# Kernel tuning notes

Measured on AMD Instinct MI355X. Metric: run time of the kernel, lower is better.

The kernel has to match this reference:

```python
import jax, jax.numpy as jnp
import numpy as np

N, C, CI, H, W = 4, 512, 256, 64, 64  # batch, in_channels, inter_channels, spatial
EPS = 1e-5


def conv1x1(x, w, b):
    # x: (N,C,H,W), w: (O,C), b: (O,)
    return jnp.einsum('nchw,oc->nohw', x, w) + b[None, :, None, None]


def setup_inputs() -> dict:
    key = jax.random.key(0)
    ks = jax.random.split(key, 11)
    s = 0.02
    return {
        'x': jax.random.normal(ks[0], (N, C, H, W), dtype=jnp.float32),
        'g_w': jax.random.normal(ks[1], (CI, C), dtype=jnp.float32) * s,
        'g_b': jax.random.normal(ks[2], (CI,), dtype=jnp.float32) * s,
        'theta_w': jax.random.normal(ks[3], (CI, C), dtype=jnp.float32) * s,
        'theta_b': jax.random.normal(ks[4], (CI,), dtype=jnp.float32) * s,
        'phi_w': jax.random.normal(ks[5], (CI, C), dtype=jnp.float32) * s,
        'phi_b': jax.random.normal(ks[6], (CI,), dtype=jnp.float32) * s,
        'wz_w': jax.random.normal(ks[7], (C, CI), dtype=jnp.float32) * s,
        'wz_b': jax.random.normal(ks[8], (C,), dtype=jnp.float32) * s,
        'bn_gamma': jax.random.normal(ks[9], (C,), dtype=jnp.float32) * 0.1 + 1.0,
        'bn_beta': jax.random.normal(ks[10], (C,), dtype=jnp.float32) * 0.1,
    }


def reference(x, g_w, g_b, theta_w, theta_b, phi_w, phi_b, wz_w, wz_b, bn_gamma, bn_beta):
    # NLBlockND.forward_self, mode='embedded', dimension=2, bn_layer=True
    n = x.shape[0]
    L = x.shape[2] * x.shape[3]  # H*W tokens
    g_x = conv1x1(x, g_w, g_b).reshape(n, CI, L)          # (N,Ci,L)
    theta_x = conv1x1(x, theta_w, theta_b).reshape(n, CI, L)
    phi_x = conv1x1(x, phi_w, phi_b).reshape(n, CI, L)
    f = jnp.einsum('ncl,ncm->nlm', theta_x, phi_x)        # (N,L,L) = theta^T @ phi
    f_div_C = jax.nn.softmax(f, axis=-1)
    y = jnp.einsum('nlm,ncm->ncl', f_div_C, g_x)          # (N,Ci,L) = (attn @ g)^T
    y = y.reshape(n, CI, x.shape[2], x.shape[3])
    w_y = conv1x1(y, wz_w, wz_b)                          # (N,C,H,W)
    # BatchNorm2d, training-mode batch statistics (biased variance)
    mean = jnp.mean(w_y, axis=(0, 2, 3), keepdims=True)
    var = jnp.var(w_y, axis=(0, 2, 3), keepdims=True)
    w_y = (w_y - mean) * jax.lax.rsqrt(var + EPS)
    w_y = w_y * bn_gamma[None, :, None, None] + bn_beta[None, :, None, None]
    return w_y + x
```

## Files before the change

### kernel.cpp

```cpp
#include <hip/hip_runtime.h>
#include <hip/hip_bf16.h>
#include <hip/hip_fp16.h>


#define NB    4
#define CDIM  512
#define CIDIM 256
#define LDIM  4096
#define BN_EPS 1e-5f

typedef unsigned short u16;
typedef __attribute__((ext_vector_type(8))) short short8;
typedef __attribute__((ext_vector_type(4))) float f32x4;
typedef __attribute__((ext_vector_type(16))) float f32x16;

#define WY_OFF    0
#define THPH_OFF  8388608
#define G_OFF     12582912
#define Y_OFF     14680064
#define WTS_OFF   16777216
#define BIAS2_OFF 17039360
#define ML_OFF    17039872
#define ST_OFF    17105408

__device__ __forceinline__ u16 f2b(float f) {
    union { float f; unsigned u; } v; v.f = f;
    return (u16)((v.u + 0x7FFFu + ((v.u >> 16) & 1u)) >> 16);
}

__device__ __forceinline__ float b2f(u16 x) {
    return __uint_as_float((unsigned)x << 16);
}

__device__ __forceinline__ unsigned pack2(float a, float b) {
    return (unsigned)f2b(a) | ((unsigned)f2b(b) << 16);
}

__device__ __forceinline__ void gl_lds16(const u16* g, u16* l) {
    __builtin_amdgcn_global_load_lds(
        (const __attribute__((address_space(1))) void*)g,
        (__attribute__((address_space(3))) void*)l, 16, 0, 0);
}

__global__ void transpose_x(const float* __restrict__ x, u16* __restrict__ xt) {
    __shared__ float tile[32][33];
    int n = blockIdx.z;
    int l0 = blockIdx.x * 32, c0 = blockIdx.y * 32;
    const float* xn = x + (size_t)n * CDIM * LDIM;
    u16* xtn = xt + (size_t)n * LDIM * CDIM;
    int tx = threadIdx.x, ty = threadIdx.y;
#pragma unroll
    for (int k = 0; k < 4; k++)
        tile[ty + 8 * k][tx] = xn[(size_t)(c0 + ty + 8 * k) * LDIM + l0 + tx];
    __syncthreads();
#pragma unroll
    for (int k = 0; k < 4; k++)
        xtn[(size_t)(l0 + ty + 8 * k) * CDIM + c0 + tx] = f2b(tile[tx][ty + 8 * k]);
}

__global__ void cast_w(const float* __restrict__ gw, const float* __restrict__ tw,
                       const float* __restrict__ pw, const float* __restrict__ zw,
                       u16* __restrict__ out) {
    int idx = blockIdx.x * 256 + threadIdx.x;
    if (idx >= 4 * 131072) return;
    int seg = idx >> 17, off = idx & 131071;
    const float* s = (seg == 0) ? gw : (seg == 1) ? tw : (seg == 2) ? pw : zw;
    out[idx] = f2b(s[off]);
}

__global__ void concat_bias(const float* __restrict__ tb, const float* __restrict__ pb,
                            float* __restrict__ out) {
    int i = blockIdx.x * 256 + threadIdx.x;
    if (i < 256) out[i] = tb[i];
    else if (i < 512) out[i] = pb[i - 256];
}

template <int BIAS_MODE, bool OUT_BF16>
__global__ __launch_bounds__(256)
void gemm_nt(const u16* __restrict__ A, const u16* __restrict__ B,
             void* __restrict__ Dv, const float* __restrict__ bias,
             int K, int lda, int ldb, int ldd,
             long batchA, long batchB, long batchD) {
    __shared__ __align__(16) u16 As[128 * 32];
    __shared__ __align__(16) u16 Bs[128 * 32];
    int z = blockIdx.z;
    A += (size_t)z * batchA;
    B += (size_t)z * batchB;

    int tid = threadIdx.x, lane = tid & 63, wave = tid >> 6;
    int n0 = blockIdx.x * 128, m0 = blockIdx.y * 128;
    int wr = wave >> 1, wc = wave & 1;

    f32x4 acc[4][4];
#pragma unroll
    for (int i = 0; i < 4; i++)
#pragma unroll
        for (int j = 0; j < 4; j++) acc[i][j] = (f32x4){0.f, 0.f, 0.f, 0.f};

    int sr = wave * 16 + (lane >> 2);
    int ss = ((lane & 3) ^ ((lane >> 2) & 3)) * 8;
    const u16* Ag0 = A + (size_t)(m0 + sr) * lda + ss;
    const u16* Ag1 = A + (size_t)(m0 + 64 + sr) * lda + ss;
    const u16* Bg0 = B + (size_t)(n0 + sr) * ldb + ss;
    const u16* Bg1 = B + (size_t)(n0 + 64 + sr) * ldb + ss;
    u16* Al0 = &As[(wave * 16) * 32];
    u16* Al1 = &As[(64 + wave * 16) * 32];
    u16* Bl0 = &Bs[(wave * 16) * 32];
    u16* Bl1 = &Bs[(64 + wave * 16) * 32];

    int koff = ((lane >> 4) ^ (lane & 3)) * 8;
    int ra = (wr * 64 + (lane & 15)) * 32 + koff;
    int rb = (wc * 64 + (lane & 15)) * 32 + koff;

    for (int k0 = 0; k0 < K; k0 += 32) {
        __syncthreads();
        gl_lds16(Ag0 + k0, Al0);
        gl_lds16(Ag1 + k0, Al1);
        gl_lds16(Bg0 + k0, Bl0);
        gl_lds16(Bg1 + k0, Bl1);
        __syncthreads();

        short8 af[4], bf[4];
#pragma unroll
        for (int mt = 0; mt < 4; mt++) af[mt] = *(const short8*)&As[ra + mt * 16 * 32];
#pragma unroll
        for (int nt = 0; nt < 4; nt++) bf[nt] = *(const short8*)&Bs[rb + nt * 16 * 32];
#pragma unroll
        for (int mt = 0; mt < 4; mt++)
#pragma unroll
            for (int nt = 0; nt < 4; nt++)
                acc[mt][nt] = __builtin_amdgcn_mfma_f32_16x16x32_bf16(
                    af[mt], bf[nt], acc[mt][nt], 0, 0, 0);
    }

#pragma unroll
    for (int mt = 0; mt < 4; mt++) {
        int mg = m0 + wr * 64 + mt * 16 + (lane >> 4) * 4;
#pragma unroll
        for (int nt = 0; nt < 4; nt++) {
            int ng = n0 + wc * 64 + nt * 16 + (lane & 15);
#pragma unroll
            for (int r = 0; r < 4; r++) {
                float v = acc[mt][nt][r];
                if (BIAS_MODE == 1) v += bias[mg + r];
                if (BIAS_MODE == 2) v += bias[ng];
                if (OUT_BF16) {
                    u16* D = (u16*)Dv + (size_t)z * batchD;
                    D[(size_t)(mg + r) * ldd + ng] = f2b(v);
                } else {
                    float* D = (float*)Dv + (size_t)z * batchD;
                    D[(size_t)(mg + r) * ldd + ng] = v;
                }
            }
        }
    }
}

__global__ __launch_bounds__(256, 2)
void flash_attn(const u16* __restrict__ THPH, const u16* __restrict__ G,
                u16* __restrict__ OPB, unsigned* __restrict__ ML4) {
    __shared__ __align__(16) u16 Ks[64 * 256];
    __shared__ __align__(16) u16 Vs[256 * 64];

    int b = blockIdx.x;
    int n = b & 3;
    int jh = (b >> 2) & 3;
    int qt = b >> 4;
    int q0 = qt * 128;

    const u16* TH = THPH + (size_t)n * LDIM * 512;
    const u16* PH = TH + 256;
    const u16* Gn = G + (size_t)n * LDIM * CIDIM;
    u16* OPh = OPB + ((size_t)jh * NB + n) * CIDIM * LDIM;
    unsigned* MLh = ML4 + ((size_t)jh * NB + n) * LDIM;

    int tid = threadIdx.x, lane = tid & 63, w = tid >> 6;
    int h = lane >> 5, lq = lane & 31, l7 = lane & 7;

    short8 qf[16];
    {
        const u16* qb = TH + (size_t)(q0 + w * 32 + lq) * 512 + h * 8;
#pragma unroll
        for (int c = 0; c < 16; c++) qf[c] = *(const short8*)(qb + c * 16);
    }

    f32x16 o[8];
#pragma unroll
    for (int i = 0; i < 8; i++)
#pragma unroll
        for (int e = 0; e < 16; e++) o[i][e] = 0.f;
    float m = -3e38f, lsum = 0.f;

    int krh = lane >> 5;
    int ksl = lane & 31;
    int vr = lane >> 3;
    int vsl = (lane & 7) ^ vr;

#define STAGE(jt_) do {                                                        \
    int j0_ = (jh * 16 + (jt_)) * 64;                                          \
    _Pragma("unroll")                                                          \
    for (int i = 0; i < 8; i++) {                                              \
        int r = w * 16 + 2 * i + krh;                                          \
        int s = ksl ^ (r & 7);                                                 \
        gl_lds16(PH + (size_t)(j0_ + r) * 512 + s * 8,                         \
                 &Ks[(w * 16 + 2 * i) * 256]);                                 \
    }                                                                          \
    _Pragma("unroll")                                                          \
    for (int i = 0; i < 8; i++) {                                              \
        int r = w * 64 + 8 * i + vr;                                           \
        gl_lds16(Gn + (size_t)r * LDIM + j0_ + vsl * 8,                        \
                 &Vs[(w * 64 + 8 * i) * 64]);                                  \
    }                                                                          \
} while (0)

#pragma unroll 1
    for (int jt = 0; jt < 16; jt++) {
        __syncthreads();
        STAGE(jt);
        __syncthreads();

        f32x16 sv[2];
#pragma unroll
        for (int t = 0; t < 2; t++) {
            f32x16 a;
#pragma unroll
            for (int e = 0; e < 16; e++) a[e] = 0.f;
#pragma unroll
            for (int c = 0; c < 16; c++) {
                int slot = (c * 2 + h) ^ l7;
                short8 ka = *(const short8*)&Ks[(t * 32 + lq) * 256 + slot * 8];
                a = __builtin_amdgcn_mfma_f32_32x32x16_bf16(ka, qf[c], a, 0, 0, 0);
            }
            sv[t] = a;
        }

        float tm = sv[0][0];
#pragma unroll
        for (int r = 1; r < 16; r++) tm = fmaxf(tm, sv[0][r]);
#pragma unroll
        for (int r = 0; r < 16; r++) tm = fmaxf(tm, sv[1][r]);
        tm = fmaxf(tm, __shfl_xor(tm, 32, 64));

        float mnew = fmaxf(m, tm);
        float al = __expf(m - mnew);
        m = mnew;
        lsum *= al;
#pragma unroll
        for (int i = 0; i < 8; i++)
#pragma unroll
            for (int e = 0; e < 16; e++) o[i][e] *= al;

        float rs = 0.f;
#pragma unroll
        for (int t = 0; t < 2; t++)
#pragma unroll
            for (int r = 0; r < 16; r++) {
                float p = __expf(sv[t][r] - m);
                sv[t][r] = p;
                rs += p;
            }
        lsum += rs + __shfl_xor(rs, 32, 64);

#pragma unroll
        for (int t = 0; t < 2; t++) {
#pragma unroll
            for (int s2 = 0; s2 < 2; s2++) {
                int st = t * 2 + s2;
                int r0 = 8 * s2;
                float e0 = sv[t][r0 + 0], e1 = sv[t][r0 + 1];
                float e2 = sv[t][r0 + 2], e3 = sv[t][r0 + 3];
                float e4 = sv[t][r0 + 4], e5 = sv[t][r0 + 5];
                float e6 = sv[t][r0 + 6], e7 = sv[t][r0 + 7];
                unsigned own_a = h ? pack2(e4, e5) : pack2(e0, e1);
                unsigned own_b = h ? pack2(e6, e7) : pack2(e2, e3);
                unsigned snd_a = h ? pack2(e0, e1) : pack2(e4, e5);
                unsigned snd_b = h ? pack2(e2, e3) : pack2(e6, e7);
                unsigned rcv_a = __shfl_xor(snd_a, 32, 64);
                unsigned rcv_b = __shfl_xor(snd_b, 32, 64);
                union { unsigned u[4]; short8 v; } pf;
                pf.u[0] = h ? rcv_a : own_a;
                pf.u[1] = h ? rcv_b : own_b;
                pf.u[2] = h ? own_a : rcv_a;
                pf.u[3] = h ? own_b : rcv_b;
                int slot = (st * 2 + h) ^ l7;
#pragma unroll
                for (int cit = 0; cit < 8; cit++) {
                    short8 va = *(const short8*)&Vs[(cit * 32 + lq) * 64 + slot * 8];
                    o[cit] = __builtin_amdgcn_mfma_f32_32x32x16_bf16(va, pf.v, o[cit], 0, 0, 0);
                }
            }
        }
    }

    int q = q0 + w * 32 + lq;
    if (h == 0) {
        unsigned pm = (unsigned)__half_as_ushort(__float2half(m));
        unsigned pl = (unsigned)__half_as_ushort(__float2half(lsum));
        MLh[q] = pm | (pl << 16);
    }
#pragma unroll
    for (int cit = 0; cit < 8; cit++)
#pragma unroll
        for (int rr = 0; rr < 16; rr++) {
            int ci = cit * 32 + (rr & 3) + 8 * (rr >> 2) + 4 * h;
            OPh[(size_t)ci * LDIM + q] = f2b(o[cit][rr]);
        }
#undef STAGE
}

__global__ void merge_y(const u16* __restrict__ OPB, const unsigned* __restrict__ ML4,
                        u16* __restrict__ Y) {
    __shared__ u16 tile[32][33];
    int nn = blockIdx.z;
    int l0 = blockIdx.x * 32, ci0 = blockIdx.y * 32;
    int tx = threadIdx.x, ty = threadIdx.y;
    int l = l0 + tx;

    float mq[4], lq[4];
#pragma unroll
    for (int q = 0; q < 4; q++) {
        unsigned u = ML4[((size_t)q * NB + nn) * LDIM + l];
        mq[q] = __half2float(__ushort_as_half((unsigned short)(u & 0xffff)));
        lq[q] = __half2float(__ushort_as_half((unsigned short)(u >> 16)));
    }
    float M = fmaxf(fmaxf(mq[0], mq[1]), fmaxf(mq[2], mq[3]));
    float wq[4];
    float den = 0.f;
#pragma unroll
    for (int q = 0; q < 4; q++) {
        wq[q] = __expf(mq[q] - M);
        den += lq[q] * wq[q];
    }
    float inv = 1.f / den;
#pragma unroll
    for (int q = 0; q < 4; q++) wq[q] *= inv;

#pragma unroll
    for (int k = 0; k < 4; k++) {
        int ci = ci0 + ty + 8 * k;
        float acc = 0.f;
#pragma unroll
        for (int q = 0; q < 4; q++)
            acc += b2f(OPB[((size_t)q * NB + nn) * CIDIM * LDIM + (size_t)ci * LDIM + l]) * wq[q];
        tile[ty + 8 * k][tx] = f2b(acc);
    }
    __syncthreads();
    u16* Yn = Y + (size_t)nn * LDIM * CIDIM;
#pragma unroll
    for (int k = 0; k < 4; k++)
        Yn[(size_t)(l0 + ty + 8 * k) * CIDIM + ci0 + tx] = tile[tx][ty + 8 * k];
}

__global__ void bn_stats_kernel(const float* __restrict__ WY, float* __restrict__ stats) {
    int o = blockIdx.x, tid = threadIdx.x, lane = tid & 63, wave = tid >> 6;
    float s = 0.f, s2 = 0.f;
    for (int n = 0; n < NB; n++) {
        const float4* p = (const float4*)(WY + (size_t)(n * CDIM + o) * LDIM);
        for (int i = tid; i < LDIM / 4; i += 256) {
            float4 v = p[i];
            s += v.x + v.y + v.z + v.w;
            s2 += v.x * v.x + v.y * v.y + v.z * v.z + v.w * v.w;
        }
    }
    for (int o2 = 32; o2 > 0; o2 >>= 1) {
        s += __shfl_xor(s, o2, 64);
        s2 += __shfl_xor(s2, o2, 64);
    }
    __shared__ float rs[4], rs2[4];
    if (lane == 0) { rs[wave] = s; rs2[wave] = s2; }
    __syncthreads();
    if (tid == 0) {
        float S = rs[0] + rs[1] + rs[2] + rs[3];
        float S2 = rs2[0] + rs2[1] + rs2[2] + rs2[3];
        const float cnt = (float)(NB * LDIM);
        float mean = S / cnt;
        float var = S2 / cnt - mean * mean;
        stats[o] = mean;
        stats[CDIM + o] = rsqrtf(var + BN_EPS);
    }
}

__global__ void bn_apply_kernel(const float* __restrict__ WY, const float* __restrict__ stats,
                                const float* __restrict__ x,
                                const float* __restrict__ gamma, const float* __restrict__ beta,
                                float* __restrict__ out) {
    int i4 = blockIdx.x * 256 + threadIdx.x;
    int o = (i4 >> 10) & (CDIM - 1);
    float m = stats[o], is = stats[CDIM + o];
    float ga = gamma[o], be = beta[o];
    float4 w = ((const float4*)WY)[i4];
    float4 xv = ((const float4*)x)[i4];
    float4 r;
    r.x = (w.x - m) * is * ga + be + xv.x;
    r.y = (w.y - m) * is * ga + be + xv.y;
    r.z = (w.z - m) * is * ga + be + xv.z;
    r.w = (w.w - m) * is * ga + be + xv.w;
    ((float4*)out)[i4] = r;
}

extern "C" void kernel_launch(void* const* d_in, const int* in_sizes, int n_in,
                              void* d_out, int out_size, void* d_ws, size_t ws_size,
                              hipStream_t stream) {
    const float* x   = (const float*)d_in[0];
    const float* gw  = (const float*)d_in[1];
    const float* gb  = (const float*)d_in[2];
    const float* tw  = (const float*)d_in[3];
    const float* tb  = (const float*)d_in[4];
    const float* pw  = (const float*)d_in[5];
    const float* pb  = (const float*)d_in[6];
    const float* zw  = (const float*)d_in[7];
    const float* zb  = (const float*)d_in[8];
    const float* bng = (const float*)d_in[9];
    const float* bnb = (const float*)d_in[10];
    float* out = (float*)d_out;
    float* ws  = (float*)d_ws;

    float*    WY   = ws + WY_OFF;
    u16*      xT   = (u16*)(ws + WY_OFF);
    u16*      OPB  = (u16*)(ws + WY_OFF);
    u16*      THPH = (u16*)(ws + THPH_OFF);
    u16*      G    = (u16*)(ws + G_OFF);
    u16*      Y    = (u16*)(ws + Y_OFF);
    u16*      WB   = (u16*)(ws + WTS_OFF);
    float*    BC   = ws + BIAS2_OFF;
    unsigned* ML4  = (unsigned*)(ws + ML_OFF);
    float*    ST   = ws + ST_OFF;

    const long LC   = (long)LDIM * CDIM;
    const long LCI  = (long)LDIM * CIDIM;
    const long L512 = (long)LDIM * 512;
    const long CL   = (long)CDIM * LDIM;

    transpose_x<<<dim3(LDIM / 32, CDIM / 32, NB), dim3(32, 8), 0, stream>>>(x, xT);
    cast_w<<<2048, 256, 0, stream>>>(gw, tw, pw, zw, WB);
    concat_bias<<<2, 256, 0, stream>>>(tb, pb, BC);

    gemm_nt<2, true><<<dim3(4, 32, NB), 256, 0, stream>>>(
        xT, WB + 131072, THPH, BC, CDIM, CDIM, CDIM, 512, LC, 0, L512);
    gemm_nt<1, true><<<dim3(32, 2, NB), 256, 0, stream>>>(
        WB, xT, G, gb, CDIM, CDIM, CDIM, LDIM, 0, LC, LCI);

    flash_attn<<<dim3(512), 256, 0, stream>>>(THPH, G, OPB, ML4);
    merge_y<<<dim3(LDIM / 32, CIDIM / 32, NB), dim3(32, 8), 0, stream>>>(OPB, ML4, Y);

    gemm_nt<1, false><<<dim3(32, 4, NB), 256, 0, stream>>>(
        WB + 393216, Y, (void*)WY, zb, CIDIM, CIDIM, CIDIM, LDIM, 0, LCI, CL);

    bn_stats_kernel<<<dim3(CDIM), 256, 0, stream>>>(WY, ST);
    bn_apply_kernel<<<dim3(NB * CDIM * LDIM / 4 / 256), 256, 0, stream>>>(
        WY, ST, x, bng, bnb, out);
}
```

Baseline: 328.7 us.

## Double-buffer K/V tiles in flash attention and skip small softmax rescales

```diff
diff --git a/kernel.cpp b/kernel.cpp
--- a/kernel.cpp
+++ b/kernel.cpp
@@ -159,8 +159,8 @@
 __global__ __launch_bounds__(256, 2)
 void flash_attn(const u16* __restrict__ THPH, const u16* __restrict__ G,
                 u16* __restrict__ OPB, unsigned* __restrict__ ML4) {
-    __shared__ __align__(16) u16 Ks[64 * 256];
-    __shared__ __align__(16) u16 Vs[256 * 64];
+    __shared__ __align__(16) u16 Ks[2][32 * 256];
+    __shared__ __align__(16) u16 Vs[2][256 * 32];
 
     int b = blockIdx.x;
     int n = b & 3;
@@ -193,103 +193,99 @@
 
     int krh = lane >> 5;
     int ksl = lane & 31;
-    int vr = lane >> 3;
-    int vsl = (lane & 7) ^ vr;
-
-#define STAGE(jt_) do {                                                        \
-    int j0_ = (jh * 16 + (jt_)) * 64;                                          \
+    int vr = lane >> 2;
+    int vsl = (lane & 3) ^ ((lane >> 3) & 3);
+
+#define STAGE(bufi, jt_) do {                                                  \
+    int j0_ = jh * 1024 + (jt_) * 32;                                          \
     _Pragma("unroll")                                                          \
-    for (int i = 0; i < 8; i++) {                                              \
-        int r = w * 16 + 2 * i + krh;                                          \
+    for (int i = 0; i < 4; i++) {                                              \
+        int r = w * 8 + 2 * i + krh;                                           \
         int s = ksl ^ (r & 7);                                                 \
         gl_lds16(PH + (size_t)(j0_ + r) * 512 + s * 8,                         \
-                 &Ks[(w * 16 + 2 * i) * 256]);                                 \
+                 &Ks[bufi][(w * 8 + 2 * i) * 256]);                            \
     }                                                                          \
     _Pragma("unroll")                                                          \
-    for (int i = 0; i < 8; i++) {                                              \
-        int r = w * 64 + 8 * i + vr;                                           \
+    for (int i = 0; i < 4; i++) {                                              \
+        int r = w * 64 + 16 * i + vr;                                          \
         gl_lds16(Gn + (size_t)r * LDIM + j0_ + vsl * 8,                        \
-                 &Vs[(w * 64 + 8 * i) * 64]);                                  \
+                 &Vs[bufi][(w * 64 + 16 * i) * 32]);                           \
     }                                                                          \
 } while (0)
 
+    STAGE(0, 0);
+    int cur = 0;
+
 #pragma unroll 1
-    for (int jt = 0; jt < 16; jt++) {
+    for (int jt = 0; jt < 32; jt++) {
         __syncthreads();
-        STAGE(jt);
-        __syncthreads();
-
-        f32x16 sv[2];
-#pragma unroll
-        for (int t = 0; t < 2; t++) {
-            f32x16 a;
-#pragma unroll
-            for (int e = 0; e < 16; e++) a[e] = 0.f;
-#pragma unroll
-            for (int c = 0; c < 16; c++) {
-                int slot = (c * 2 + h) ^ l7;
-                short8 ka = *(const short8*)&Ks[(t * 32 + lq) * 256 + slot * 8];
-                a = __builtin_amdgcn_mfma_f32_32x32x16_bf16(ka, qf[c], a, 0, 0, 0);
+        if (jt + 1 < 32) STAGE(cur ^ 1, jt + 1);
+
+        const u16* kb = Ks[cur];
+        const u16* vb = Vs[cur];
+
+        f32x16 sv;
+#pragma unroll
+        for (int e = 0; e < 16; e++) sv[e] = 0.f;
+#pragma unroll
+        for (int c = 0; c < 16; c++) {
+            int slot = (c * 2 + h) ^ l7;
+            short8 ka = *(const short8*)&kb[lq * 256 + slot * 8];
+            sv = __builtin_amdgcn_mfma_f32_32x32x16_bf16(ka, qf[c], sv, 0, 0, 0);
+        }
+
+        float tm = sv[0];
+#pragma unroll
+        for (int r = 1; r < 16; r++) tm = fmaxf(tm, sv[r]);
+        tm = fmaxf(tm, __shfl_xor(tm, 32, 64));
+
+        if (!__all(tm <= m + 8.0f)) {
+            float mnew = fmaxf(m, tm);
+            float al = __expf(m - mnew);
+            m = mnew;
+            lsum *= al;
+#pragma unroll
+            for (int i = 0; i < 8; i++)
+#pragma unroll
+                for (int e = 0; e < 16; e++) o[i][e] *= al;
+        }
+
+        float rs = 0.f;
+#pragma unroll
+        for (int r = 0; r < 16; r++) {
+            float p = __expf(sv[r] - m);
+            sv[r] = p;
+            rs += p;
+        }
+        lsum += rs + __shfl_xor(rs, 32, 64);
+
+#pragma unroll
+        for (int st = 0; st < 2; st++) {
+            int r0 = 8 * st;
+            float e0 = sv[r0 + 0], e1 = sv[r0 + 1];
+            float e2 = sv[r0 + 2], e3 = sv[r0 + 3];
+            float e4 = sv[r0 + 4], e5 = sv[r0 + 5];
+            float e6 = sv[r0 + 6], e7 = sv[r0 + 7];
+            unsigned own_a = h ? pack2(e4, e5) : pack2(e0, e1);
+            unsigned own_b = h ? pack2(e6, e7) : pack2(e2, e3);
+            unsigned snd_a = h ? pack2(e0, e1) : pack2(e4, e5);
+            unsigned snd_b = h ? pack2(e2, e3) : pack2(e6, e7);
+            unsigned rcv_a = __shfl_xor(snd_a, 32, 64);
+            unsigned rcv_b = __shfl_xor(snd_b, 32, 64);
+            union { unsigned u[4]; short8 v; } pf;
+            pf.u[0] = h ? rcv_a : own_a;
+            pf.u[1] = h ? rcv_b : own_b;
+            pf.u[2] = h ? own_a : rcv_a;
+            pf.u[3] = h ? own_b : rcv_b;
+#pragma unroll
+            for (int cit = 0; cit < 8; cit++) {
+                int row = cit * 32 + lq;
+                int slot = (st * 2 + h) ^ ((lq >> 1) & 3);
+                short8 va = *(const short8*)&vb[row * 32 + slot * 8];
+                o[cit] = __builtin_amdgcn_mfma_f32_32x32x16_bf16(va, pf.v, o[cit], 0, 0, 0);
             }
-            sv[t] = a;
-        }
-
-        float tm = sv[0][0];
-#pragma unroll
-        for (int r = 1; r < 16; r++) tm = fmaxf(tm, sv[0][r]);
-#pragma unroll
-        for (int r = 0; r < 16; r++) tm = fmaxf(tm, sv[1][r]);
-        tm = fmaxf(tm, __shfl_xor(tm, 32, 64));
-
-        float mnew = fmaxf(m, tm);
-        float al = __expf(m - mnew);
-        m = mnew;
-        lsum *= al;
-#pragma unroll
-        for (int i = 0; i < 8; i++)
-#pragma unroll
-            for (int e = 0; e < 16; e++) o[i][e] *= al;
-
-        float rs = 0.f;
-#pragma unroll
-        for (int t = 0; t < 2; t++)
-#pragma unroll
-            for (int r = 0; r < 16; r++) {
-                float p = __expf(sv[t][r] - m);
-                sv[t][r] = p;
-                rs += p;
-            }
-        lsum += rs + __shfl_xor(rs, 32, 64);
-
-#pragma unroll
-        for (int t = 0; t < 2; t++) {
-#pragma unroll
-            for (int s2 = 0; s2 < 2; s2++) {
-                int st = t * 2 + s2;
-                int r0 = 8 * s2;
-                float e0 = sv[t][r0 + 0], e1 = sv[t][r0 + 1];
-                float e2 = sv[t][r0 + 2], e3 = sv[t][r0 + 3];
-                float e4 = sv[t][r0 + 4], e5 = sv[t][r0 + 5];
-                float e6 = sv[t][r0 + 6], e7 = sv[t][r0 + 7];
-                unsigned own_a = h ? pack2(e4, e5) : pack2(e0, e1);
-                unsigned own_b = h ? pack2(e6, e7) : pack2(e2, e3);
-                unsigned snd_a = h ? pack2(e0, e1) : pack2(e4, e5);
-                unsigned snd_b = h ? pack2(e2, e3) : pack2(e6, e7);
-                unsigned rcv_a = __shfl_xor(snd_a, 32, 64);
-                unsigned rcv_b = __shfl_xor(snd_b, 32, 64);
-                union { unsigned u[4]; short8 v; } pf;
-                pf.u[0] = h ? rcv_a : own_a;
-                pf.u[1] = h ? rcv_b : own_b;
-                pf.u[2] = h ? own_a : rcv_a;
-                pf.u[3] = h ? own_b : rcv_b;
-                int slot = (st * 2 + h) ^ l7;
-#pragma unroll
-                for (int cit = 0; cit < 8; cit++) {
-                    short8 va = *(const short8*)&Vs[(cit * 32 + lq) * 64 + slot * 8];
-                    o[cit] = __builtin_amdgcn_mfma_f32_32x32x16_bf16(va, pf.v, o[cit], 0, 0, 0);
-                }
-            }
-        }
+        }
+        cur ^= 1;
     }
 
     int q = q0 + w * 32 + lq;
```

Result: faster. 295.4 us (-10.1%).
